# Optimization experiments

Measured on AMD Instinct MI355X. Metric: run time of the kernel, lower is better.

The kernel has to match this reference:

```python
import jax, jax.numpy as jnp
import numpy as np

B, L, H, F, K, NBINS, T = 32, 512, 512, 512, 3, 256, 4096
EPS = 1e-8  # RMSNorm epsilon
PAD = (K - 1) // 2  # =1, matches both conv paddings in the torch module


def _conv1d(x, w, b):
    # x: [B, L, Cin], w: [K, Cin, Cout]
    return jax.lax.conv_general_dilated(
        x, w, window_strides=(1,), padding=[(PAD, PAD)],
        dimension_numbers=('NLC', 'LIO', 'NLC')) + b


def _rms(x, g):
    return g * x / (jnp.sqrt(jnp.mean(x * x, axis=-1, keepdims=True)) + EPS)


def _vpred(x, mask, w1, b1, g1, w2, b2, g2, wl, bl):
    h = _rms(jax.nn.relu(_conv1d(x, w1, b1)), g1)
    h = _rms(jax.nn.relu(_conv1d(h, w2, b2)), g2)
    out = (h @ wl + bl)[..., 0]  # [B, L]
    return jnp.where(mask, 0.0, out)


def _proj(x, w1, b1, w2, b2):
    return jax.nn.relu(jax.nn.relu(x @ w1 + b1) @ w2 + b2)


def _length_regulate(x, dur, max_len):
    # Vectorized equivalent of LengthRegulator: repeat phoneme i dur[b,i] times, pad to max_len.
    cum = jnp.cumsum(dur, axis=1)               # [B, L]
    mel_len = cum[:, -1]                        # [B]
    t = jnp.arange(max_len)                     # [T]
    idx = jax.vmap(lambda c: jnp.searchsorted(c, t, side='right'))(cum)  # [B, T]
    idx = jnp.minimum(idx, x.shape[1] - 1)
    out = jnp.take_along_axis(x, idx[:, :, None], axis=1)  # [B, T, H]
    valid = (t[None, :] < mel_len[:, None])
    return out * valid[:, :, None].astype(x.dtype), mel_len


def setup_inputs() -> dict:
    key = jax.random.key(0)
    ks = iter(jax.random.split(key, 64))
    n = lambda *s: jax.random.normal(next(ks), s, jnp.float32) * 0.05
    inp = {}
    inp['x'] = jax.random.normal(next(ks), (B, L, H), jnp.float32)
    inp['embedding'] = jax.random.normal(next(ks), (B, L, H), jnp.float32)
    inp['src_mask'] = jnp.zeros((B, L), bool)
    inp['duration_target'] = jax.random.randint(next(ks), (B, L), 0, 9, jnp.int32)
    inp['pitch_target'] = jax.random.normal(next(ks), (B, L), jnp.float32)
    inp['energy_target'] = jax.random.normal(next(ks), (B, L), jnp.float32)
    inp['max_len'] = T
    for p in ['dur', 'pit', 'eng']:
        inp[p + '_w1'] = n(K, H, F); inp[p + '_b1'] = jnp.zeros(F, jnp.float32)
        inp[p + '_g1'] = jnp.ones(F, jnp.float32)
        inp[p + '_w2'] = n(K, F, F); inp[p + '_b2'] = jnp.zeros(F, jnp.float32)
        inp[p + '_g2'] = jnp.ones(F, jnp.float32)
        inp[p + '_wl'] = n(F, 1); inp[p + '_bl'] = jnp.zeros(1, jnp.float32)
    for p in ['pp', 'ep', 'sp']:
        inp[p + '_w1'] = n(H, H); inp[p + '_b1'] = jnp.zeros(H, jnp.float32)
        inp[p + '_w2'] = n(H, H); inp[p + '_b2'] = jnp.zeros(H, jnp.float32)
    inp['pitch_bins'] = jnp.linspace(-3.0, 3.0, NBINS - 1)
    inp['energy_bins'] = jnp.linspace(-3.0, 3.0, NBINS - 1)
    inp['pitch_emb'] = n(NBINS, H)
    inp['energy_emb'] = n(NBINS, H)
    return inp


def reference(x, embedding, src_mask, duration_target, pitch_target, energy_target, max_len,
              dur_w1, dur_b1, dur_g1, dur_w2, dur_b2, dur_g2, dur_wl, dur_bl,
              pit_w1, pit_b1, pit_g1, pit_w2, pit_b2, pit_g2, pit_wl, pit_bl,
              eng_w1, eng_b1, eng_g1, eng_w2, eng_b2, eng_g2, eng_wl, eng_bl,
              pp_w1, pp_b1, pp_w2, pp_b2,
              ep_w1, ep_b1, ep_w2, ep_b2,
              sp_w1, sp_b1, sp_w2, sp_b2,
              pitch_bins, energy_bins, pitch_emb, energy_emb):
    log_dur = _vpred(x, src_mask, dur_w1, dur_b1, dur_g1, dur_w2, dur_b2, dur_g2, dur_wl, dur_bl)
    pit_pred = _vpred(x + _proj(embedding, pp_w1, pp_b1, pp_w2, pp_b2), src_mask,
                      pit_w1, pit_b1, pit_g1, pit_w2, pit_b2, pit_g2, pit_wl, pit_bl)
    pitch_embedding = pitch_emb[jnp.searchsorted(pitch_bins, pitch_target)]  # torch.bucketize right=False == side='left'
    eng_pred = _vpred(x + _proj(embedding, ep_w1, ep_b1, ep_w2, ep_b2), src_mask,
                      eng_w1, eng_b1, eng_g1, eng_w2, eng_b2, eng_g2, eng_wl, eng_bl)
    energy_embedding = energy_emb[jnp.searchsorted(energy_bins, energy_target)]
    xo = x + energy_embedding + pitch_embedding + _proj(embedding, sp_w1, sp_b1, sp_w2, sp_b2)
    out, mel_len = _length_regulate(xo, duration_target, max_len)
    return (out, pit_pred, eng_pred, log_dur, mel_len)
```

## Files before the change

kernel.cpp:

```cpp
#include <hip/hip_runtime.h>

#define Bv    32
#define Lv    512
#define Hv    512
#define Fv    512
#define Tv    4096
#define Mv    (Bv*Lv)
#define NBINSv 256

#define OUT_OFF 0
#define PIT_OFF (Bv*(size_t)Tv*Hv)
#define ENG_OFF (PIT_OFF + Mv)
#define DUR_OFF (ENG_OFF + Mv)
#define MEL_OFF (DUR_OFF + Mv)

typedef unsigned short ushort;
typedef __attribute__((ext_vector_type(8))) short   bf16x8;
typedef __attribute__((ext_vector_type(4))) float   f32x4;
typedef __attribute__((ext_vector_type(8))) unsigned short u16x8;

__device__ __forceinline__ float b2f(ushort u) {
    union { float f; unsigned u; } x; x.u = ((unsigned)u) << 16; return x.f;
}
__device__ __forceinline__ ushort f2b(float f) {
    union { float f; unsigned u; } x; x.f = f;
    unsigned r = x.u + 0x7fffu + ((x.u >> 16) & 1u);
    return (ushort)(r >> 16);
}

#define GLL16(g, l) __builtin_amdgcn_global_load_lds( \
    (const __attribute__((address_space(1))) void*)(g), \
    (__attribute__((address_space(3))) void*)(l), 16, 0, 0)

#define FENCE() asm volatile("" ::: "memory")
#define BAR() do { FENCE(); __builtin_amdgcn_s_barrier(); FENCE(); } while (0)
#define VMCNT(N) asm volatile("s_waitcnt vmcnt(" #N ")" ::: "memory")

template<int NZ> struct GArgs {
    const ushort* A[NZ];
    const ushort* W[NZ];
    const float*  bias[NZ];
    ushort*       C[NZ];
};
struct RmsArgs   { const ushort* h[3]; const float* g[3]; ushort* o[3]; };
struct RlArgs    { const ushort* h[3]; const float* g[3]; const float* wl[3]; const float* bl[3]; };
struct TransArgs { const float* src[6]; ushort* dst[6]; };
struct ConvArgs  { const float* src[2]; ushort* dst[2]; };

#define MFMA_Q(IOFF, JOFF)                                               \
    do {                                                                 \
        __builtin_amdgcn_s_setprio(1);                                   \
        _Pragma("unroll")                                                \
        for (int s_ = 0; s_ < 2; ++s_)                                   \
            _Pragma("unroll")                                            \
            for (int i_ = 0; i_ < 4; ++i_)                               \
                _Pragma("unroll")                                        \
                for (int j_ = 0; j_ < 2; ++j_)                           \
                    acc[(IOFF) + i_][(JOFF) + j_] =                      \
                        __builtin_amdgcn_mfma_f32_16x16x32_bf16(         \
                            a_f[i_][s_], b_f[(JOFF) + j_][s_],           \
                            acc[(IOFF) + i_][(JOFF) + j_], 0, 0, 0);     \
        __builtin_amdgcn_s_setprio(0);                                   \
    } while (0)

template<int NTAPS, int EPI, int NZ>
__global__ __launch_bounds__(512) void gemm256_kernel(
    GArgs<NZ> ga, const float* __restrict__ res, const float* __restrict__ pe,
    const float* __restrict__ ee, const int* __restrict__ idxp,
    const int* __restrict__ idxe, const ushort* __restrict__ zp)
{
    constexpr int KTOT = NTAPS * 512;
    constexpr int NT   = KTOT / 64;
    const int z = (NZ > 1) ? blockIdx.z : 0;
    const ushort* __restrict__ A    = ga.A[z];
    const ushort* __restrict__ Bt   = ga.W[z];
    const float*  __restrict__ bias = ga.bias[z];
    ushort*       __restrict__ C    = ga.C[z];

    __shared__ ushort As[2][256][64];
    __shared__ ushort Bs[2][256][64];

    const int tid  = threadIdx.x;
    const int n0   = blockIdx.x * 256;
    const int m0   = blockIdx.y * 256;
    const int lane = tid & 63;
    const int w    = tid >> 6;
    const int wr   = w >> 2;
    const int wc   = w & 3;
    const int lr   = lane & 15;
    const int q    = lane >> 4;

    const int srow = tid >> 3;
    const int scol = ((tid & 7) ^ (srow & 7)) << 3;

    auto stageA = [&](int buf, int h, int kt) {
        const int tap = (NTAPS == 3) ? (kt >> 3) : 0;
        const int kin = (NTAPS == 3) ? ((kt & 7) << 6) : (kt << 6);
        #pragma unroll
        for (int r = 0; r < 2; ++r) {
            const int row = h * 128 + r * 64 + srow;
            const int m   = m0 + row;
            const ushort* src;
            if (NTAPS == 3) {
                const int ls = (m & (Lv - 1)) + tap - 1;
                src = ((unsigned)ls < (unsigned)Lv)
                    ? A + (size_t)(m + tap - 1) * 512 + kin + scol
                    : zp;
            } else {
                src = A + (size_t)m * 512 + kin + scol;
            }
            GLL16(src, ((ushort*)As) + buf * 16384 + h * 8192 + r * 4096 + tid * 8);
        }
    };
    auto stageB = [&](int buf, int h, int kt) {
        #pragma unroll
        for (int r = 0; r < 2; ++r) {
            const int n = n0 + h * 128 + r * 64 + srow;
            const ushort* src = Bt + (size_t)n * KTOT + kt * 64 + scol;
            GLL16(src, ((ushort*)Bs) + buf * 16384 + h * 8192 + r * 4096 + tid * 8);
        }
    };

    const int ca0 = ((q * 16) ^ ((lr & 7) << 4)) >> 1;
    const int ca1 = ((64 + q * 16) ^ ((lr & 7) << 4)) >> 1;
    auto readA = [&](int buf, int i8, int s) -> bf16x8 {
        const int rm = ((i8 < 4) ? (wr * 64 + i8 * 16)
                                 : (128 + wr * 64 + (i8 - 4) * 16)) + lr;
        return *(const bf16x8*)(((const ushort*)As) + buf * 16384 + rm * 64 + (s ? ca1 : ca0));
    };
    auto readB = [&](int buf, int j, int s) -> bf16x8 {
        const int rn = ((j < 2) ? (wc * 32 + j * 16)
                                : (128 + wc * 32 + (j - 2) * 16)) + lr;
        return *(const bf16x8*)(((const ushort*)Bs) + buf * 16384 + rn * 64 + (s ? ca1 : ca0));
    };

    f32x4 acc[8][4];
    #pragma unroll
    for (int i = 0; i < 8; ++i)
        #pragma unroll
        for (int j = 0; j < 4; ++j) {
            f32x4 zz = {0.f, 0.f, 0.f, 0.f};
            acc[i][j] = zz;
        }
    bf16x8 a_f[4][2], b_f[4][2];

    stageA(0, 0, 0); stageA(0, 1, 0);
    stageB(0, 0, 0); stageB(0, 1, 0);
    stageA(1, 0, 1);
    stageB(1, 0, 1); stageB(1, 1, 1);
    VMCNT(6);
    BAR();

    #pragma unroll 1
    for (int t = 0; t < NT; t += 2) {
        const bool pf = (t + 2 < NT);
        #pragma unroll
        for (int i = 0; i < 4; ++i) { a_f[i][0] = readA(0, i, 0); a_f[i][1] = readA(0, i, 1); }
        #pragma unroll
        for (int j = 0; j < 2; ++j) { b_f[j][0] = readB(0, j, 0); b_f[j][1] = readB(0, j, 1); }
        stageA(1, 1, t + 1);
        BAR();
        MFMA_Q(0, 0);
        BAR();
        #pragma unroll
        for (int j = 2; j < 4; ++j) { b_f[j][0] = readB(0, j, 0); b_f[j][1] = readB(0, j, 1); }
        if (pf) stageA(0, 0, t + 2);
        BAR();
        MFMA_Q(0, 2);
        BAR();
        #pragma unroll
        for (int i = 0; i < 4; ++i) { a_f[i][0] = readA(0, 4 + i, 0); a_f[i][1] = readA(0, 4 + i, 1); }
        if (pf) stageB(0, 0, t + 2);
        BAR();
        MFMA_Q(4, 0);
        BAR();
        if (pf) { stageB(0, 1, t + 2); VMCNT(6); }
        else    { VMCNT(0); }
        BAR();
        MFMA_Q(4, 2);
        BAR();
        #pragma unroll
        for (int i = 0; i < 4; ++i) { a_f[i][0] = readA(1, i, 0); a_f[i][1] = readA(1, i, 1); }
        #pragma unroll
        for (int j = 0; j < 2; ++j) { b_f[j][0] = readB(1, j, 0); b_f[j][1] = readB(1, j, 1); }
        if (pf) stageA(0, 1, t + 2);
        BAR();
        MFMA_Q(0, 0);
        BAR();
        #pragma unroll
        for (int j = 2; j < 4; ++j) { b_f[j][0] = readB(1, j, 0); b_f[j][1] = readB(1, j, 1); }
        if (pf) stageA(1, 0, t + 3);
        BAR();
        MFMA_Q(0, 2);
        BAR();
        #pragma unroll
        for (int i = 0; i < 4; ++i) { a_f[i][0] = readA(1, 4 + i, 0); a_f[i][1] = readA(1, 4 + i, 1); }
        if (pf) stageB(1, 0, t + 3);
        BAR();
        MFMA_Q(4, 0);
        BAR();
        if (pf) stageB(1, 1, t + 3);
        VMCNT(6);
        BAR();
        MFMA_Q(4, 2);
        BAR();
    }

    int epi = EPI;
    if (EPI == 3) epi = (z == 2) ? 2 : 1;
    #pragma unroll
    for (int i = 0; i < 8; ++i) {
        const int mrow = (i < 4) ? (wr * 64 + i * 16) : (128 + wr * 64 + (i - 4) * 16);
        #pragma unroll
        for (int r = 0; r < 4; ++r) {
            const int m = m0 + mrow + q * 4 + r;
            const size_t ro = (size_t)m * 512;
            int ip = 0, ie = 0;
            if (EPI >= 2 && epi == 2) { ip = idxp[m]; ie = idxe[m]; }
            #pragma unroll
            for (int j = 0; j < 4; ++j) {
                const int ncol = (j < 2) ? (wc * 32 + j * 16) : (128 + wc * 32 + (j - 2) * 16);
                const int n = n0 + ncol + lr;
                float v = acc[i][j][r] + bias[n];
                v = fmaxf(v, 0.f);
                if (EPI != 0 && epi >= 1) v += res[ro + n];
                if (EPI >= 2 && epi == 2) v += pe[(size_t)ip * 512 + n] + ee[(size_t)ie * 512 + n];
                C[ro + n] = f2b(v);
            }
        }
    }
}

__global__ __launch_bounds__(256) void convert_kernel(ConvArgs ca)
{
    const float* __restrict__ X  = ca.src[blockIdx.y];
    ushort*      __restrict__ Xb = ca.dst[blockIdx.y];
    const size_t i = (size_t)blockIdx.x * 256 + threadIdx.x;
    const float4 a = ((const float4*)X)[2 * i];
    const float4 b = ((const float4*)X)[2 * i + 1];
    u16x8 o;
    o[0] = f2b(a.x); o[1] = f2b(a.y); o[2] = f2b(a.z); o[3] = f2b(a.w);
    o[4] = f2b(b.x); o[5] = f2b(b.y); o[6] = f2b(b.z); o[7] = f2b(b.w);
    *(u16x8*)(Xb + i * 8) = o;
}

__global__ __launch_bounds__(256) void transpose_kernel(TransArgs ta, int Ktot)
{
    const float* __restrict__ W  = ta.src[blockIdx.z];
    ushort*      __restrict__ Wt = ta.dst[blockIdx.z];
    __shared__ float t[32][33];
    const int k0 = blockIdx.x * 32, n0 = blockIdx.y * 32;
    const int r = threadIdx.x >> 5, c = threadIdx.x & 31;
    #pragma unroll
    for (int rr = 0; rr < 4; ++rr)
        t[r + rr * 8][c] = W[(size_t)(k0 + r + rr * 8) * 512 + n0 + c];
    __syncthreads();
    #pragma unroll
    for (int rr = 0; rr < 4; ++rr)
        Wt[(size_t)(n0 + r + rr * 8) * Ktot + k0 + c] = f2b(t[c][r + rr * 8]);
}

__global__ __launch_bounds__(128) void rms_kernel(RmsArgs ra)
{
    const int z = blockIdx.y;
    const int row = blockIdx.x;
    const int tid = threadIdx.x;
    const ushort* __restrict__ h = ra.h[z];
    const ushort4 hv = ((const ushort4*)(h + (size_t)row * 512))[tid];
    const float v0 = b2f(hv.x), v1 = b2f(hv.y), v2 = b2f(hv.z), v3 = b2f(hv.w);
    float ss = v0 * v0 + v1 * v1 + v2 * v2 + v3 * v3;
    #pragma unroll
    for (int off = 32; off; off >>= 1) ss += __shfl_down(ss, off, 64);
    __shared__ float p[2];
    if ((tid & 63) == 0) p[tid >> 6] = ss;
    __syncthreads();
    const float tot = p[0] + p[1];
    const float inv = 1.f / (sqrtf(tot * (1.f / 512.f)) + 1e-8f);
    const float4 gv = ((const float4*)ra.g[z])[tid];
    ushort4 ov;
    ov.x = f2b(gv.x * v0 * inv); ov.y = f2b(gv.y * v1 * inv);
    ov.z = f2b(gv.z * v2 * inv); ov.w = f2b(gv.w * v3 * inv);
    ((ushort4*)(ra.o[z] + (size_t)row * 512))[tid] = ov;
}

__global__ __launch_bounds__(256) void rmslin_kernel(
    RlArgs ra, const unsigned char* __restrict__ mask, float* __restrict__ predbase)
{
    const int z = blockIdx.y;
    const int wave = threadIdx.x >> 6, lane = threadIdx.x & 63;
    const int row = blockIdx.x * 4 + wave;
    const ushort* __restrict__ h = ra.h[z];
    const bf16x8 hv = *(const bf16x8*)(h + (size_t)row * 512 + lane * 8);
    const float4 g0 = *(const float4*)(ra.g[z] + lane * 8);
    const float4 g1 = *(const float4*)(ra.g[z] + lane * 8 + 4);
    const float4 w0 = *(const float4*)(ra.wl[z] + lane * 8);
    const float4 w1 = *(const float4*)(ra.wl[z] + lane * 8 + 4);
    float hf[8];
    #pragma unroll
    for (int t = 0; t < 8; ++t) hf[t] = b2f((ushort)hv[t]);
    float ss = 0.f, sgw = 0.f;
    #pragma unroll
    for (int t = 0; t < 8; ++t) ss += hf[t] * hf[t];
    sgw += hf[0]*g0.x*w0.x + hf[1]*g0.y*w0.y + hf[2]*g0.z*w0.z + hf[3]*g0.w*w0.w;
    sgw += hf[4]*g1.x*w1.x + hf[5]*g1.y*w1.y + hf[6]*g1.z*w1.z + hf[7]*g1.w*w1.w;
    #pragma unroll
    for (int off = 32; off; off >>= 1) {
        ss  += __shfl_down(ss,  off, 64);
        sgw += __shfl_down(sgw, off, 64);
    }
    if (lane == 0) {
        const float inv = 1.f / (sqrtf(ss * (1.f / 512.f)) + 1e-8f);
        predbase[(size_t)z * Mv + row] = mask[row] ? 0.f : (sgw * inv + ra.bl[z][0]);
    }
}

__global__ __launch_bounds__(256) void idx_kernel(
    const float* __restrict__ pt, const float* __restrict__ et,
    const float* __restrict__ pbins, const float* __restrict__ ebins,
    int* __restrict__ idxp, int* __restrict__ idxe)
{
    __shared__ float pb[NBINSv - 1], ebn[NBINSv - 1];
    const int tid = threadIdx.x;
    if (tid < NBINSv - 1) { pb[tid] = pbins[tid]; ebn[tid] = ebins[tid]; }
    __syncthreads();
    const int m = blockIdx.x * 256 + tid;
    const float pv = pt[m], ev = et[m];
    int lo = 0, hi = NBINSv - 1;
    while (lo < hi) { int mid = (lo + hi) >> 1; if (pb[mid] < pv) lo = mid + 1; else hi = mid; }
    idxp[m] = lo;
    lo = 0; hi = NBINSv - 1;
    while (lo < hi) { int mid = (lo + hi) >> 1; if (ebn[mid] < ev) lo = mid + 1; else hi = mid; }
    idxe[m] = lo;
}

__global__ __launch_bounds__(512) void cumsum_kernel(
    const int* __restrict__ dur, int* __restrict__ cum,
    int* __restrict__ melint, float* __restrict__ melout)
{
    __shared__ int s[Lv];
    const int b = blockIdx.x, tid = threadIdx.x;
    s[tid] = dur[b * Lv + tid];
    __syncthreads();
    for (int off = 1; off < Lv; off <<= 1) {
        int t = (tid >= off) ? s[tid - off] : 0;
        __syncthreads();
        s[tid] += t;
        __syncthreads();
    }
    cum[b * Lv + tid] = s[tid];
    if (tid == Lv - 1) { melint[b] = s[tid]; melout[b] = (float)s[tid]; }
}

__global__ __launch_bounds__(256) void tmap_kernel(
    const int* __restrict__ cum, const int* __restrict__ melint,
    int* __restrict__ tmap)
{
    const int bt = blockIdx.x * 256 + threadIdx.x;
    const int b = bt >> 12;
    const int t = bt & (Tv - 1);
    const int* c = cum + b * Lv;
    int lo = 0, hi = Lv;
    while (lo < hi) { int mid = (lo + hi) >> 1; if (c[mid] <= t) lo = mid + 1; else hi = mid; }
    tmap[bt] = (t < melint[b]) ? (b * Lv + min(lo, Lv - 1)) : -1;
}

__global__ __launch_bounds__(128) void regulate_kernel(
    const ushort* __restrict__ xo, const int* __restrict__ tmap,
    float* __restrict__ out)
{
    const int bt = blockIdx.x;
    const int src = tmap[bt];
    float4 v = make_float4(0.f, 0.f, 0.f, 0.f);
    if (src >= 0) {
        const ushort4 u = ((const ushort4*)(xo + (size_t)src * 512))[threadIdx.x];
        v.x = b2f(u.x); v.y = b2f(u.y); v.z = b2f(u.z); v.w = b2f(u.w);
    }
    ((float4*)(out + (size_t)bt * 512))[threadIdx.x] = v;
}

extern "C" void kernel_launch(void* const* d_in, const int* in_sizes, int n_in,
                              void* d_out, int out_size, void* d_ws, size_t ws_size,
                              hipStream_t stream)
{
    const float* x    = (const float*)d_in[0];
    const float* emb  = (const float*)d_in[1];
    const unsigned char* mask = (const unsigned char*)d_in[2];
    const int*   durt = (const int*)d_in[3];
    const float* pt   = (const float*)d_in[4];
    const float* et   = (const float*)d_in[5];
    const float* dw1 = (const float*)d_in[7],  *db1 = (const float*)d_in[8],
               * dg1 = (const float*)d_in[9],  *dw2 = (const float*)d_in[10],
               * db2 = (const float*)d_in[11], *dg2 = (const float*)d_in[12],
               * dwl = (const float*)d_in[13], *dbl = (const float*)d_in[14];
    const float* pw1 = (const float*)d_in[15], *pb1 = (const float*)d_in[16],
               * pg1 = (const float*)d_in[17], *pw2 = (const float*)d_in[18],
               * pb2 = (const float*)d_in[19], *pg2 = (const float*)d_in[20],
               * pwl = (const float*)d_in[21], *pbl = (const float*)d_in[22];
    const float* ew1 = (const float*)d_in[23], *eb1 = (const float*)d_in[24],
               * eg1 = (const float*)d_in[25], *ew2 = (const float*)d_in[26],
               * eb2 = (const float*)d_in[27], *eg2 = (const float*)d_in[28],
               * ewl = (const float*)d_in[29], *ebl = (const float*)d_in[30];
    const float* ppw1 = (const float*)d_in[31], *ppb1 = (const float*)d_in[32],
               * ppw2 = (const float*)d_in[33], *ppb2 = (const float*)d_in[34];
    const float* epw1 = (const float*)d_in[35], *epb1 = (const float*)d_in[36],
               * epw2 = (const float*)d_in[37], *epb2 = (const float*)d_in[38];
    const float* spw1 = (const float*)d_in[39], *spb1 = (const float*)d_in[40],
               * spw2 = (const float*)d_in[41], *spb2 = (const float*)d_in[42];
    const float* pbins = (const float*)d_in[43];
    const float* ebins = (const float*)d_in[44];
    const float* pemb  = (const float*)d_in[45];
    const float* eemb  = (const float*)d_in[46];

    float* outf = (float*)d_out;

    int*    cum    = (int*)d_ws;
    int*    melint = cum + 16384;
    int*    idxp   = melint + 64;
    int*    idxe   = idxp + 16384;
    ushort* zp     = (ushort*)(idxe + 16384);
    int*    tmap   = idxe + 16448;
    ushort* xob    = (ushort*)((float*)d_ws + 262144);

    #define OBUF(i) ((ushort*)(outf + (size_t)(i) * 4194304))
    ushort* xb  = OBUF(0);   ushort* eb  = OBUF(1);
    ushort* pA0 = OBUF(2);   ushort* pA1 = OBUF(3);  ushort* pA2 = OBUF(4);
    ushort* xp  = OBUF(5);   ushort* xe  = OBUF(6);
    ushort* c0  = OBUF(7);   ushort* c1  = OBUF(8);  ushort* c2  = OBUF(9);
    ushort* r0  = OBUF(10);  ushort* r1  = OBUF(11); ushort* r2  = OBUF(12);
    ushort* wt[12];
    {
        size_t off = 13ull * 4194304;
        for (int i = 0; i < 6; ++i)  { wt[i] = (ushort*)(outf + off); off += 393216; }
        for (int i = 6; i < 12; ++i) { wt[i] = (ushort*)(outf + off); off += 131072; }
    }

    hipMemsetAsync(zp, 0, 64, stream);

    { ConvArgs ca = {{x, emb}, {xb, eb}};
      convert_kernel<<<dim3(4096, 2), 256, 0, stream>>>(ca); }
    { TransArgs ta = {{dw1, dw2, pw1, pw2, ew1, ew2}, {wt[0], wt[1], wt[2], wt[3], wt[4], wt[5]}};
      transpose_kernel<<<dim3(48, 16, 6), 256, 0, stream>>>(ta, 1536); }
    { TransArgs ta = {{ppw1, ppw2, epw1, epw2, spw1, spw2},
                      {wt[6], wt[7], wt[8], wt[9], wt[10], wt[11]}};
      transpose_kernel<<<dim3(16, 16, 6), 256, 0, stream>>>(ta, 512); }

    idx_kernel<<<Mv / 256, 256, 0, stream>>>(pt, et, pbins, ebins, idxp, idxe);
    cumsum_kernel<<<Bv, Lv, 0, stream>>>(durt, cum, melint, outf + MEL_OFF);
    tmap_kernel<<<Bv * Tv / 256, 256, 0, stream>>>(cum, melint, tmap);

    const dim3 g3(Fv / 256, Mv / 256, 3);

    { GArgs<3> a = {{eb, eb, eb}, {wt[6], wt[8], wt[10]}, {ppb1, epb1, spb1}, {pA0, pA1, pA2}};
      gemm256_kernel<1, 0, 3><<<g3, 512, 0, stream>>>(a, nullptr, nullptr, nullptr,
                                                      nullptr, nullptr, zp); }
    { GArgs<3> a = {{pA0, pA1, pA2}, {wt[7], wt[9], wt[11]}, {ppb2, epb2, spb2}, {xp, xe, xob}};
      gemm256_kernel<1, 3, 3><<<g3, 512, 0, stream>>>(a, x, pemb, eemb,
                                                      idxp, idxe, zp); }

    { GArgs<3> a = {{xp, xe, xb}, {wt[2], wt[4], wt[0]}, {pb1, eb1, db1}, {c0, c1, c2}};
      gemm256_kernel<3, 0, 3><<<g3, 512, 0, stream>>>(a, nullptr, nullptr, nullptr,
                                                      nullptr, nullptr, zp); }
    { RmsArgs ra = {{c0, c1, c2}, {pg1, eg1, dg1}, {r0, r1, r2}};
      rms_kernel<<<dim3(Mv, 3), 128, 0, stream>>>(ra); }
    { GArgs<3> a = {{r0, r1, r2}, {wt[3], wt[5], wt[1]}, {pb2, eb2, db2}, {c0, c1, c2}};
      gemm256_kernel<3, 0, 3><<<g3, 512, 0, stream>>>(a, nullptr, nullptr, nullptr,
                                                      nullptr, nullptr, zp); }
    { RlArgs ra = {{c0, c1, c2}, {pg2, eg2, dg2}, {pwl, ewl, dwl}, {pbl, ebl, dbl}};
      rmslin_kernel<<<dim3(Mv / 4, 3), 256, 0, stream>>>(ra, mask, outf + PIT_OFF); }

    regulate_kernel<<<Bv * Tv, 128, 0, stream>>>(xob, tmap, outf + OUT_OFF);
}
```

Baseline: 893.2 us.

## Shrink GEMM tile to 128x256 with triple-buffered LDS pipeline

```diff
diff --git a/kernel.cpp b/kernel.cpp
--- a/kernel.cpp
+++ b/kernel.cpp
@@ -47,24 +47,24 @@
 struct TransArgs { const float* src[6]; ushort* dst[6]; };
 struct ConvArgs  { const float* src[2]; ushort* dst[2]; };
 
-#define MFMA_Q(IOFF, JOFF)                                               \
+#define MFMA_C(IOFF)                                                     \
     do {                                                                 \
         __builtin_amdgcn_s_setprio(1);                                   \
         _Pragma("unroll")                                                \
         for (int s_ = 0; s_ < 2; ++s_)                                   \
             _Pragma("unroll")                                            \
-            for (int i_ = 0; i_ < 4; ++i_)                               \
+            for (int i_ = 0; i_ < 2; ++i_)                               \
                 _Pragma("unroll")                                        \
-                for (int j_ = 0; j_ < 2; ++j_)                           \
-                    acc[(IOFF) + i_][(JOFF) + j_] =                      \
+                for (int j_ = 0; j_ < 4; ++j_)                           \
+                    acc[(IOFF) + i_][j_] =                               \
                         __builtin_amdgcn_mfma_f32_16x16x32_bf16(         \
-                            a_f[i_][s_], b_f[(JOFF) + j_][s_],           \
-                            acc[(IOFF) + i_][(JOFF) + j_], 0, 0, 0);     \
+                            a_f[i_][s_], b_f[j_][s_],                    \
+                            acc[(IOFF) + i_][j_], 0, 0, 0);              \
         __builtin_amdgcn_s_setprio(0);                                   \
     } while (0)
 
 template<int NTAPS, int EPI, int NZ>
-__global__ __launch_bounds__(512) void gemm256_kernel(
+__global__ __launch_bounds__(512) void gemm128_kernel(
     GArgs<NZ> ga, const float* __restrict__ res, const float* __restrict__ pe,
     const float* __restrict__ ee, const int* __restrict__ idxp,
     const int* __restrict__ idxe, const ushort* __restrict__ zp)
@@ -77,12 +77,12 @@
     const float*  __restrict__ bias = ga.bias[z];
     ushort*       __restrict__ C    = ga.C[z];
 
-    __shared__ ushort As[2][256][64];
-    __shared__ ushort Bs[2][256][64];
+    __shared__ ushort As[3][128][64];
+    __shared__ ushort Bs[3][256][64];
 
     const int tid  = threadIdx.x;
     const int n0   = blockIdx.x * 256;
-    const int m0   = blockIdx.y * 256;
+    const int m0   = blockIdx.y * 128;
     const int lane = tid & 63;
     const int w    = tid >> 6;
     const int wr   = w >> 2;
@@ -93,12 +93,12 @@
     const int srow = tid >> 3;
     const int scol = ((tid & 7) ^ (srow & 7)) << 3;
 
-    auto stageA = [&](int buf, int h, int kt) {
+    auto stageA = [&](int buf, int kt) {
         const int tap = (NTAPS == 3) ? (kt >> 3) : 0;
         const int kin = (NTAPS == 3) ? ((kt & 7) << 6) : (kt << 6);
         #pragma unroll
         for (int r = 0; r < 2; ++r) {
-            const int row = h * 128 + r * 64 + srow;
+            const int row = r * 64 + srow;
             const int m   = m0 + row;
             const ushort* src;
             if (NTAPS == 3) {
@@ -109,7 +109,7 @@
             } else {
                 src = A + (size_t)m * 512 + kin + scol;
             }
-            GLL16(src, ((ushort*)As) + buf * 16384 + h * 8192 + r * 4096 + tid * 8);
+            GLL16(src, ((ushort*)As) + buf * 8192 + r * 4096 + tid * 8);
         }
     };
     auto stageB = [&](int buf, int h, int kt) {
@@ -121,106 +121,68 @@
         }
     };
 
-    const int ca0 = ((q * 16) ^ ((lr & 7) << 4)) >> 1;
-    const int ca1 = ((64 + q * 16) ^ ((lr & 7) << 4)) >> 1;
-    auto readA = [&](int buf, int i8, int s) -> bf16x8 {
-        const int rm = ((i8 < 4) ? (wr * 64 + i8 * 16)
-                                 : (128 + wr * 64 + (i8 - 4) * 16)) + lr;
-        return *(const bf16x8*)(((const ushort*)As) + buf * 16384 + rm * 64 + (s ? ca1 : ca0));
+    const int ca0 = ((q) ^ (lr & 7)) << 3;
+    const int ca1 = ((4 + q) ^ (lr & 7)) << 3;
+    auto readA = [&](int buf, int i, int s) -> bf16x8 {
+        const int rm = wr * 64 + i * 16 + lr;
+        return *(const bf16x8*)(((const ushort*)As) + buf * 8192 + rm * 64 + (s ? ca1 : ca0));
     };
     auto readB = [&](int buf, int j, int s) -> bf16x8 {
-        const int rn = ((j < 2) ? (wc * 32 + j * 16)
-                                : (128 + wc * 32 + (j - 2) * 16)) + lr;
+        const int rn = wc * 64 + j * 16 + lr;
         return *(const bf16x8*)(((const ushort*)Bs) + buf * 16384 + rn * 64 + (s ? ca1 : ca0));
     };
 
-    f32x4 acc[8][4];
-    #pragma unroll
-    for (int i = 0; i < 8; ++i)
+    f32x4 acc[4][4];
+    #pragma unroll
+    for (int i = 0; i < 4; ++i)
         #pragma unroll
         for (int j = 0; j < 4; ++j) {
             f32x4 zz = {0.f, 0.f, 0.f, 0.f};
             acc[i][j] = zz;
         }
-    bf16x8 a_f[4][2], b_f[4][2];
-
-    stageA(0, 0, 0); stageA(0, 1, 0);
-    stageB(0, 0, 0); stageB(0, 1, 0);
-    stageA(1, 0, 1);
-    stageB(1, 0, 1); stageB(1, 1, 1);
+    bf16x8 a_f[2][2], b_f[4][2];
+
+    stageB(0, 0, 0); stageB(0, 1, 0); stageA(0, 0);
+    stageB(1, 0, 1); stageB(1, 1, 1); stageA(1, 1);
     VMCNT(6);
     BAR();
 
+    int p = 0;
     #pragma unroll 1
-    for (int t = 0; t < NT; t += 2) {
+    for (int t = 0; t < NT; ++t) {
         const bool pf = (t + 2 < NT);
-        #pragma unroll
-        for (int i = 0; i < 4; ++i) { a_f[i][0] = readA(0, i, 0); a_f[i][1] = readA(0, i, 1); }
-        #pragma unroll
-        for (int j = 0; j < 2; ++j) { b_f[j][0] = readB(0, j, 0); b_f[j][1] = readB(0, j, 1); }
-        stageA(1, 1, t + 1);
+        const int pw = (p == 0) ? 2 : p - 1;
+        #pragma unroll
+        for (int i = 0; i < 2; ++i) { a_f[i][0] = readA(p, i, 0); a_f[i][1] = readA(p, i, 1); }
+        #pragma unroll
+        for (int j = 0; j < 4; ++j) { b_f[j][0] = readB(p, j, 0); b_f[j][1] = readB(p, j, 1); }
+        if (pf) { stageB(pw, 0, t + 2); stageB(pw, 1, t + 2); stageA(pw, t + 2); }
         BAR();
-        MFMA_Q(0, 0);
+        MFMA_C(0);
         BAR();
         #pragma unroll
-        for (int j = 2; j < 4; ++j) { b_f[j][0] = readB(0, j, 0); b_f[j][1] = readB(0, j, 1); }
-        if (pf) stageA(0, 0, t + 2);
-        BAR();
-        MFMA_Q(0, 2);
-        BAR();
-        #pragma unroll
-        for (int i = 0; i < 4; ++i) { a_f[i][0] = readA(0, 4 + i, 0); a_f[i][1] = readA(0, 4 + i, 1); }
-        if (pf) stageB(0, 0, t + 2);
-        BAR();
-        MFMA_Q(4, 0);
-        BAR();
-        if (pf) { stageB(0, 1, t + 2); VMCNT(6); }
+        for (int i = 0; i < 2; ++i) { a_f[i][0] = readA(p, 2 + i, 0); a_f[i][1] = readA(p, 2 + i, 1); }
+        if (pf) { VMCNT(6); }
         else    { VMCNT(0); }
         BAR();
-        MFMA_Q(4, 2);
+        MFMA_C(2);
         BAR();
-        #pragma unroll
-        for (int i = 0; i < 4; ++i) { a_f[i][0] = readA(1, i, 0); a_f[i][1] = readA(1, i, 1); }
-        #pragma unroll
-        for (int j = 0; j < 2; ++j) { b_f[j][0] = readB(1, j, 0); b_f[j][1] = readB(1, j, 1); }
-        if (pf) stageA(0, 1, t + 2);
-        BAR();
-        MFMA_Q(0, 0);
-        BAR();
-        #pragma unroll
-        for (int j = 2; j < 4; ++j) { b_f[j][0] = readB(1, j, 0); b_f[j][1] = readB(1, j, 1); }
-        if (pf) stageA(1, 0, t + 3);
-        BAR();
-        MFMA_Q(0, 2);
-        BAR();
-        #pragma unroll
-        for (int i = 0; i < 4; ++i) { a_f[i][0] = readA(1, 4 + i, 0); a_f[i][1] = readA(1, 4 + i, 1); }
-        if (pf) stageB(1, 0, t + 3);
-        BAR();
-        MFMA_Q(4, 0);
-        BAR();
-        if (pf) stageB(1, 1, t + 3);
-        VMCNT(6);
-        BAR();
-        MFMA_Q(4, 2);
-        BAR();
+        p = (p == 2) ? 0 : p + 1;
     }
 
     int epi = EPI;
     if (EPI == 3) epi = (z == 2) ? 2 : 1;
     #pragma unroll
-    for (int i = 0; i < 8; ++i) {
-        const int mrow = (i < 4) ? (wr * 64 + i * 16) : (128 + wr * 64 + (i - 4) * 16);
+    for (int i = 0; i < 4; ++i) {
         #pragma unroll
         for (int r = 0; r < 4; ++r) {
-            const int m = m0 + mrow + q * 4 + r;
+            const int m = m0 + wr * 64 + i * 16 + q * 4 + r;
             const size_t ro = (size_t)m * 512;
             int ip = 0, ie = 0;
             if (EPI >= 2 && epi == 2) { ip = idxp[m]; ie = idxe[m]; }
             #pragma unroll
             for (int j = 0; j < 4; ++j) {
-                const int ncol = (j < 2) ? (wc * 32 + j * 16) : (128 + wc * 32 + (j - 2) * 16);
-                const int n = n0 + ncol + lr;
+                const int n = n0 + wc * 64 + j * 16 + lr;
                 float v = acc[i][j][r] + bias[n];
                 v = fmaxf(v, 0.f);
                 if (EPI != 0 && epi >= 1) v += res[ro + n];
@@ -448,22 +410,22 @@
     cumsum_kernel<<<Bv, Lv, 0, stream>>>(durt, cum, melint, outf + MEL_OFF);
     tmap_kernel<<<Bv * Tv / 256, 256, 0, stream>>>(cum, melint, tmap);
 
-    const dim3 g3(Fv / 256, Mv / 256, 3);
+    const dim3 g3(Fv / 256, Mv / 128, 3);
 
     { GArgs<3> a = {{eb, eb, eb}, {wt[6], wt[8], wt[10]}, {ppb1, epb1, spb1}, {pA0, pA1, pA2}};
-      gemm256_kernel<1, 0, 3><<<g3, 512, 0, stream>>>(a, nullptr, nullptr, nullptr,
+      gemm128_kernel<1, 0, 3><<<g3, 512, 0, stream>>>(a, nullptr, nullptr, nullptr,
                                                       nullptr, nullptr, zp); }
     { GArgs<3> a = {{pA0, pA1, pA2}, {wt[7], wt[9], wt[11]}, {ppb2, epb2, spb2}, {xp, xe, xob}};
-      gemm256_kernel<1, 3, 3><<<g3, 512, 0, stream>>>(a, x, pemb, eemb,
+      gemm128_kernel<1, 3, 3><<<g3, 512, 0, stream>>>(a, x, pemb, eemb,
                                                       idxp, idxe, zp); }
 
     { GArgs<3> a = {{xp, xe, xb}, {wt[2], wt[4], wt[0]}, {pb1, eb1, db1}, {c0, c1, c2}};
-      gemm256_kernel<3, 0, 3><<<g3, 512, 0, stream>>>(a, nullptr, nullptr, nullptr,
+      gemm128_kernel<3, 0, 3><<<g3, 512, 0, stream>>>(a, nullptr, nullptr, nullptr,
                                                       nullptr, nullptr, zp); }
     { RmsArgs ra = {{c0, c1, c2}, {pg1, eg1, dg1}, {r0, r1, r2}};
       rms_kernel<<<dim3(Mv, 3), 128, 0, stream>>>(ra); }
     { GArgs<3> a = {{r0, r1, r2}, {wt[3], wt[5], wt[1]}, {pb2, eb2, db2}, {c0, c1, c2}};
-      gemm256_kernel<3, 0, 3><<<g3, 512, 0, stream>>>(a, nullptr, nullptr, nullptr,
+      gemm128_kernel<3, 0, 3><<<g3, 512, 0, stream>>>(a, nullptr, nullptr, nullptr,
                                                       nullptr, nullptr, zp); }
     { RlArgs ra = {{c0, c1, c2}, {pg2, eg2, dg2}, {pwl, ewl, dwl}, {pbl, ebl, dbl}};
       rmslin_kernel<<<dim3(Mv / 4, 3), 256, 0, stream>>>(ra, mask, outf + PIT_OFF); }
```

Result: faster. 866.0 us (-3.0%).
